# Performance work log

Hardware: AMD Instinct MI355X
Metric: run time of the kernel (lower is better)

Reference implementation:

```python
import jax, jax.numpy as jnp
import numpy as np

B, D, H, O = 16384, 256, 64, 256


def setup_inputs() -> dict:
    key = jax.random.key(0)
    ks = jax.random.split(key, 7)
    s1 = 1.0  # Linear(1,H): fan_in=1 -> U(-1,1)
    sH = 1.0 / np.sqrt(H)
    sD = 1.0 / np.sqrt(D)
    return {
        "x": jax.random.normal(ks[0], (B, D), dtype=jnp.float32),
        "W1": jax.random.uniform(ks[1], (D, H), jnp.float32, -s1, s1),
        "b1": jax.random.uniform(ks[2], (D, H), jnp.float32, -s1, s1),
        "W2": jax.random.uniform(ks[3], (D, H), jnp.float32, -sH, sH),
        "b2": jax.random.uniform(ks[4], (D,), jnp.float32, -sH, sH),
        "Wc": jax.random.uniform(ks[5], (O, D), jnp.float32, -sD, sD),
        "bc": jax.random.uniform(ks[6], (O,), jnp.float32, -sD, sD),
    }


def reference(x, W1, b1, W2, b2, Wc, bc):
    # Per-feature tiny MLP, batched over the feature axis D.
    # hidden: [B, D, H]
    h = jax.nn.relu(x[:, :, None] * W1[None, :, :] + b1[None, :, :])
    # collapse hidden -> scalar per feature: [B, D]
    u = jnp.einsum("bdh,dh->bd", h, W2) + b2[None, :]
    # combiner Linear(D, O)
    return u @ Wc.T + bc[None, :]
```

## Files before the change

### kernel.cpp

```cpp
#include <hip/hip_runtime.h>
#include <hip/hip_bf16.h>

#define B_N 16384
#define D_N 256
#define H_N 64
#define O_N 256

typedef unsigned int u32;
typedef unsigned short u16;
typedef __attribute__((ext_vector_type(2))) float f32x2;
typedef __attribute__((ext_vector_type(4))) float f32x4;
typedef __attribute__((ext_vector_type(8))) short short8;
typedef __attribute__((ext_vector_type(4))) short short4v;
typedef __attribute__((ext_vector_type(4))) u32 uint4v;
typedef __attribute__((ext_vector_type(2))) u32 uint2v;

__device__ u32 g_WB[D_N * H_N];
__device__ u32 g_W2p[D_N * H_N / 2];
__device__ u16 g_Wcb[O_N * D_N];

static __device__ __forceinline__ u16 f2bf(float f) {
  u32 v = __float_as_uint(f);
  return (u16)((v + 0x7fffu + ((v >> 16) & 1u)) >> 16);
}

static __device__ __forceinline__ void dma16(const u32* g, u32* l) {
  __builtin_amdgcn_global_load_lds(
      (const __attribute__((address_space(1))) u32*)g,
      (__attribute__((address_space(3))) u32*)l, 16, 0, 0);
}

__global__ __launch_bounds__(256) void prep(
    const float* __restrict__ W1, const float* __restrict__ b1,
    const float* __restrict__ W2, const float* __restrict__ Wc) {
  const int t = blockIdx.x * 256 + threadIdx.x;
  const int d = t >> 6, h = t & 63;
  g_WB[d * 64 + (h ^ ((d & 7) << 2))] =
      ((u32)f2bf(W1[t]) << 16) | (u32)f2bf(b1[t]);
  if ((h & 1) == 0) {
    g_W2p[d * 32 + ((h >> 1) ^ ((d & 7) << 1))] =
        (u32)f2bf(W2[t]) | ((u32)f2bf(W2[t + 1]) << 16);
  }
  const int i = t * 4;
  const f32x4 v = *reinterpret_cast<const f32x4*>(Wc + i);
  short4v s;
#pragma unroll
  for (int q = 0; q < 4; ++q) s[q] = (short)f2bf(v[q]);
  *reinterpret_cast<short4v*>(g_Wcb + i) = s;
}

__global__ __launch_bounds__(256, 2) void kan_fused(
    const float* __restrict__ x, const float* __restrict__ b2,
    const float* __restrict__ bc, float* __restrict__ out) {
  __shared__ u32 wbs[64 * 64];
  __shared__ u32 w2p[64 * 32];
  __shared__ u16 uT[16 * 256];

  const int tid = threadIdx.x;
  const int dl  = tid & 63;
  const int wv  = tid >> 6;
  const int b0  = blockIdx.x * 16;

  const int wswzb = (dl & 7) << 4;

  for (int c = 0; c < 4; ++c) {
    const int d0 = c * 64, drow = d0 + dl;
    __syncthreads();

    const u32* wbg = g_WB  + d0 * 64;
    const u32* w2g = g_W2p + d0 * 32;
#pragma unroll
    for (int i = 0; i < 4; ++i)
      dma16(wbg + (wv * 4 + i) * 256 + dl * 4, wbs + (wv * 4 + i) * 256);
#pragma unroll
    for (int i = 0; i < 2; ++i)
      dma16(w2g + (wv * 2 + i) * 256 + dl * 4, w2p + (wv * 2 + i) * 256);

    f32x2 xp[2], accp[2];
#pragma unroll
    for (int p = 0; p < 2; ++p) {
      const int row = b0 + wv * 4 + 2 * p;
      xp[p]   = f32x2{x[row * D_N + drow], x[(row + 1) * D_N + drow]};
      accp[p] = f32x2{0.f, 0.f};
    }
    const float b2v = b2[drow];
    __syncthreads();

    const char* wbbase = (const char*)wbs + dl * 256;
    const char* w2base = (const char*)w2p + dl * 128;
#pragma unroll
    for (int h0 = 0; h0 < H_N; h0 += 4) {
      const int wb_off = (h0 << 2) ^ wswzb;
      const uint4v wb4 = *(const uint4v*)(wbbase + wb_off);
      const uint2v w2w = *(const uint2v*)(w2base + (wb_off >> 1));
#pragma unroll
      for (int k = 0; k < 4; ++k) {
        const float w1f = __uint_as_float(wb4[k] & 0xffff0000u);
        const float b1f = __uint_as_float(wb4[k] << 16);
        const u32 w2word = w2w[k >> 1];
        const float w2f = __uint_as_float((k & 1) ? (w2word & 0xffff0000u)
                                                  : (w2word << 16));
        const f32x2 w1v = {w1f, w1f}, b1v = {b1f, b1f}, w2v = {w2f, w2f};
#pragma unroll
        for (int p = 0; p < 2; ++p) {
          f32x2 tv = __builtin_elementwise_fma(xp[p], w1v, b1v);
          tv = __builtin_elementwise_max(tv, f32x2{0.f, 0.f});
          accp[p] = __builtin_elementwise_fma(tv, w2v, accp[p]);
        }
      }
    }
#pragma unroll
    for (int p = 0; p < 2; ++p)
#pragma unroll
      for (int e = 0; e < 2; ++e) {
        const int row = wv * 4 + 2 * p + e;
        int byte = row * 512 + drow * 2;
        byte ^= (row & 7) << 4;
        *(u16*)((char*)uT + byte) = f2bf(accp[p][e] + b2v);
      }
  }
  __syncthreads();

  const int n0   = wv * 64;
  const int mrow = dl & 15;
  const int kgrp = dl >> 4;

  f32x4 acc2[4];
#pragma unroll
  for (int j = 0; j < 4; ++j) acc2[j] = (f32x4)(0.f);

#pragma unroll
  for (int ks = 0; ks < 8; ++ks) {
    const int k0 = ks * 32 + kgrp * 8;
    int byte = mrow * 512 + k0 * 2;
    byte ^= (mrow & 7) << 4;
    const short8 afrag = *reinterpret_cast<const short8*>(
        reinterpret_cast<const char*>(uT) + byte);
    short8 bfrag[4];
#pragma unroll
    for (int j = 0; j < 4; ++j)
      bfrag[j] = *reinterpret_cast<const short8*>(
          g_Wcb + (n0 + j * 16 + mrow) * D_N + k0);
#pragma unroll
    for (int j = 0; j < 4; ++j)
      acc2[j] = __builtin_amdgcn_mfma_f32_16x16x32_bf16(
          afrag, bfrag[j], acc2[j], 0, 0, 0);
  }

#pragma unroll
  for (int j = 0; j < 4; ++j) {
    const int colg = n0 + j * 16 + mrow;
    const float bcv = bc[colg];
#pragma unroll
    for (int q = 0; q < 4; ++q) {
      const int rowg = b0 + kgrp * 4 + q;
      out[rowg * O_N + colg] = acc2[j][q] + bcv;
    }
  }
}

extern "C" void kernel_launch(void* const* d_in, const int* in_sizes, int n_in,
                              void* d_out, int out_size, void* d_ws, size_t ws_size,
                              hipStream_t stream) {
  const float* x  = (const float*)d_in[0];
  const float* W1 = (const float*)d_in[1];
  const float* b1 = (const float*)d_in[2];
  const float* W2 = (const float*)d_in[3];
  const float* b2 = (const float*)d_in[4];
  const float* Wc = (const float*)d_in[5];
  const float* bc = (const float*)d_in[6];
  float* out = (float*)d_out;

  prep<<<dim3(D_N * H_N / 256), dim3(256), 0, stream>>>(W1, b1, W2, Wc);
  kan_fused<<<dim3(B_N / 16), dim3(256), 0, stream>>>(x, b2, bc, out);
}
```

Baseline: 116.0 us.

## Switch per-feature MLP to packed fp16 math with register-resident weights

```diff
diff --git a/kernel.cpp b/kernel.cpp
--- a/kernel.cpp
+++ b/kernel.cpp
@@ -1,5 +1,6 @@
 #include <hip/hip_runtime.h>
 #include <hip/hip_bf16.h>
+#include <hip/hip_fp16.h>
 
 #define B_N 16384
 #define D_N 256
@@ -8,119 +9,112 @@
 
 typedef unsigned int u32;
 typedef unsigned short u16;
-typedef __attribute__((ext_vector_type(2))) float f32x2;
+typedef _Float16 f16;
+typedef __attribute__((ext_vector_type(2))) _Float16 f16x2;
+typedef __attribute__((ext_vector_type(8))) _Float16 f16x8;
 typedef __attribute__((ext_vector_type(4))) float f32x4;
-typedef __attribute__((ext_vector_type(8))) short short8;
-typedef __attribute__((ext_vector_type(4))) short short4v;
 typedef __attribute__((ext_vector_type(4))) u32 uint4v;
-typedef __attribute__((ext_vector_type(2))) u32 uint2v;
+typedef __attribute__((ext_vector_type(4))) u16 u16x4;
 
-__device__ u32 g_WB[D_N * H_N];
-__device__ u32 g_W2p[D_N * H_N / 2];
-__device__ u16 g_Wcb[O_N * D_N];
+__device__ uint4v g_W1p[8 * 256];
+__device__ uint4v g_B1p[8 * 256];
+__device__ uint4v g_W2p[8 * 256];
+__device__ __attribute__((aligned(16))) u16 g_Wch[O_N * D_N];
 
-static __device__ __forceinline__ u16 f2bf(float f) {
-  u32 v = __float_as_uint(f);
-  return (u16)((v + 0x7fffu + ((v >> 16) & 1u)) >> 16);
+union HU { f16 h; u16 b; };
+
+static __device__ __forceinline__ u32 packh2(float a, float b) {
+  f16x2 p = {(f16)a, (f16)b};
+  return __builtin_bit_cast(u32, p);
+}
+static __device__ __forceinline__ u16 f16b(float a) {
+  HU u; u.h = (f16)a; return u.b;
+}
+static __device__ __forceinline__ f16x2 ash2(u32 w) {
+  return __builtin_bit_cast(f16x2, w);
 }
 
-static __device__ __forceinline__ void dma16(const u32* g, u32* l) {
-  __builtin_amdgcn_global_load_lds(
-      (const __attribute__((address_space(1))) u32*)g,
-      (__attribute__((address_space(3))) u32*)l, 16, 0, 0);
-}
+#if __has_builtin(__builtin_amdgcn_fdot2)
+#define FDOT2(a, b, c) __builtin_amdgcn_fdot2((a), (b), (c), false)
+#else
+#define FDOT2(a, b, c) \
+  fmaf((float)(a)[0], (float)(b)[0], fmaf((float)(a)[1], (float)(b)[1], (c)))
+#endif
 
 __global__ __launch_bounds__(256) void prep(
     const float* __restrict__ W1, const float* __restrict__ b1,
     const float* __restrict__ W2, const float* __restrict__ Wc) {
-  const int t = blockIdx.x * 256 + threadIdx.x;
-  const int d = t >> 6, h = t & 63;
-  g_WB[d * 64 + (h ^ ((d & 7) << 2))] =
-      ((u32)f2bf(W1[t]) << 16) | (u32)f2bf(b1[t]);
+  const int u = blockIdx.x * 256 + threadIdx.x;
+  const int d = u >> 6, h = u & 63;
   if ((h & 1) == 0) {
-    g_W2p[d * 32 + ((h >> 1) ^ ((d & 7) << 1))] =
-        (u32)f2bf(W2[t]) | ((u32)f2bf(W2[t + 1]) << 16);
+    const int j = h >> 1;
+    const int idx = ((j >> 2) * 256 + d) * 4 + (j & 3);
+    ((u32*)g_W1p)[idx] = packh2(W1[u], W1[u + 1]);
+    ((u32*)g_B1p)[idx] = packh2(b1[u], b1[u + 1]);
+    ((u32*)g_W2p)[idx] = packh2(W2[u], W2[u + 1]);
   }
-  const int i = t * 4;
-  const f32x4 v = *reinterpret_cast<const f32x4*>(Wc + i);
-  short4v s;
+  const int i4 = u * 4;
+  const f32x4 v = *reinterpret_cast<const f32x4*>(Wc + i4);
+  u16x4 s;
 #pragma unroll
-  for (int q = 0; q < 4; ++q) s[q] = (short)f2bf(v[q]);
-  *reinterpret_cast<short4v*>(g_Wcb + i) = s;
+  for (int q = 0; q < 4; ++q) s[q] = f16b(v[q]);
+  *reinterpret_cast<u16x4*>(g_Wch + i4) = s;
 }
 
-__global__ __launch_bounds__(256, 2) void kan_fused(
+__global__ __launch_bounds__(256, 3) void kan_fused(
     const float* __restrict__ x, const float* __restrict__ b2,
     const float* __restrict__ bc, float* __restrict__ out) {
-  __shared__ u32 wbs[64 * 64];
-  __shared__ u32 w2p[64 * 32];
   __shared__ u16 uT[16 * 256];
 
-  const int tid = threadIdx.x;
-  const int dl  = tid & 63;
-  const int wv  = tid >> 6;
-  const int b0  = blockIdx.x * 16;
+  const int t  = threadIdx.x;
+  const int b0 = blockIdx.x * 16;
 
-  const int wswzb = (dl & 7) << 4;
+  uint4v w1r[8], b1r[8], w2r[8];
+#pragma unroll
+  for (int i = 0; i < 8; ++i) {
+    w1r[i] = g_W1p[i * 256 + t];
+    b1r[i] = g_B1p[i * 256 + t];
+    w2r[i] = g_W2p[i * 256 + t];
+  }
+  const float b2v = b2[t];
 
-  for (int c = 0; c < 4; ++c) {
-    const int d0 = c * 64, drow = d0 + dl;
-    __syncthreads();
-
-    const u32* wbg = g_WB  + d0 * 64;
-    const u32* w2g = g_W2p + d0 * 32;
 #pragma unroll
-    for (int i = 0; i < 4; ++i)
-      dma16(wbg + (wv * 4 + i) * 256 + dl * 4, wbs + (wv * 4 + i) * 256);
+  for (int g = 0; g < 2; ++g) {
+    f16x2 xx[8];
+    float acc[8];
 #pragma unroll
-    for (int i = 0; i < 2; ++i)
-      dma16(w2g + (wv * 2 + i) * 256 + dl * 4, w2p + (wv * 2 + i) * 256);
-
-    f32x2 xp[2], accp[2];
+    for (int r = 0; r < 8; ++r) {
+      const float xv = x[(b0 + g * 8 + r) * D_N + t];
+      xx[r] = (f16x2){(f16)xv, (f16)xv};
+      acc[r] = 0.f;
+    }
 #pragma unroll
-    for (int p = 0; p < 2; ++p) {
-      const int row = b0 + wv * 4 + 2 * p;
-      xp[p]   = f32x2{x[row * D_N + drow], x[(row + 1) * D_N + drow]};
-      accp[p] = f32x2{0.f, 0.f};
-    }
-    const float b2v = b2[drow];
-    __syncthreads();
-
-    const char* wbbase = (const char*)wbs + dl * 256;
-    const char* w2base = (const char*)w2p + dl * 128;
+    for (int i = 0; i < 8; ++i) {
 #pragma unroll
-    for (int h0 = 0; h0 < H_N; h0 += 4) {
-      const int wb_off = (h0 << 2) ^ wswzb;
-      const uint4v wb4 = *(const uint4v*)(wbbase + wb_off);
-      const uint2v w2w = *(const uint2v*)(w2base + (wb_off >> 1));
+      for (int q = 0; q < 4; ++q) {
+        const f16x2 w1 = ash2(w1r[i][q]);
+        const f16x2 bb = ash2(b1r[i][q]);
+        const f16x2 w2 = ash2(w2r[i][q]);
 #pragma unroll
-      for (int k = 0; k < 4; ++k) {
-        const float w1f = __uint_as_float(wb4[k] & 0xffff0000u);
-        const float b1f = __uint_as_float(wb4[k] << 16);
-        const u32 w2word = w2w[k >> 1];
-        const float w2f = __uint_as_float((k & 1) ? (w2word & 0xffff0000u)
-                                                  : (w2word << 16));
-        const f32x2 w1v = {w1f, w1f}, b1v = {b1f, b1f}, w2v = {w2f, w2f};
-#pragma unroll
-        for (int p = 0; p < 2; ++p) {
-          f32x2 tv = __builtin_elementwise_fma(xp[p], w1v, b1v);
-          tv = __builtin_elementwise_max(tv, f32x2{0.f, 0.f});
-          accp[p] = __builtin_elementwise_fma(tv, w2v, accp[p]);
+        for (int r = 0; r < 8; ++r) {
+          f16x2 tv = __builtin_elementwise_fma(xx[r], w1, bb);
+          tv = __builtin_elementwise_max(tv, (f16x2){(f16)0.f, (f16)0.f});
+          acc[r] = FDOT2(tv, w2, acc[r]);
         }
       }
     }
 #pragma unroll
-    for (int p = 0; p < 2; ++p)
-#pragma unroll
-      for (int e = 0; e < 2; ++e) {
-        const int row = wv * 4 + 2 * p + e;
-        int byte = row * 512 + drow * 2;
-        byte ^= (row & 7) << 4;
-        *(u16*)((char*)uT + byte) = f2bf(accp[p][e] + b2v);
-      }
+    for (int r = 0; r < 8; ++r) {
+      const int row = g * 8 + r;
+      int byte = row * 512 + t * 2;
+      byte ^= (row & 7) << 4;
+      *(u16*)((char*)uT + byte) = f16b(acc[r] + b2v);
+    }
   }
   __syncthreads();
 
+  const int wv   = t >> 6;
+  const int dl   = t & 63;
   const int n0   = wv * 64;
   const int mrow = dl & 15;
   const int kgrp = dl >> 4;
@@ -134,17 +128,14 @@
     const int k0 = ks * 32 + kgrp * 8;
     int byte = mrow * 512 + k0 * 2;
     byte ^= (mrow & 7) << 4;
-    const short8 afrag = *reinterpret_cast<const short8*>(
-        reinterpret_cast<const char*>(uT) + byte);
-    short8 bfrag[4];
+    const f16x8 afrag = *reinterpret_cast<const f16x8*>((const char*)uT + byte);
 #pragma unroll
-    for (int j = 0; j < 4; ++j)
-      bfrag[j] = *reinterpret_cast<const short8*>(
-          g_Wcb + (n0 + j * 16 + mrow) * D_N + k0);
-#pragma unroll
-    for (int j = 0; j < 4; ++j)
-      acc2[j] = __builtin_amdgcn_mfma_f32_16x16x32_bf16(
-          afrag, bfrag[j], acc2[j], 0, 0, 0);
+    for (int j = 0; j < 4; ++j) {
+      const f16x8 bfrag = *reinterpret_cast<const f16x8*>(
+          g_Wch + (n0 + j * 16 + mrow) * D_N + k0);
+      acc2[j] = __builtin_amdgcn_mfma_f32_16x16x32_f16(afrag, bfrag, acc2[j],
+                                                       0, 0, 0);
+    }
   }
 
 #pragma unroll
```

Result: faster. 103.7 us (-10.6%).
